# Kernel tuning notes

Measured on AMD Instinct MI355X. Metric: run time of the kernel, lower is better.

Reference implementation:

```python
import jax, jax.numpy as jnp
import numpy as np

N = 4096
IN_F = 512
OUT_F = 64
N_HEADS = 8
ALPHA = 0.2
NEG_INF = -9e15


def setup_inputs() -> dict:
    key = jax.random.key(0)
    k1, k2, k3, k4 = jax.random.split(key, 4)
    h = jax.random.normal(k1, (N, IN_F), dtype=jnp.float32)
    adj = jax.random.randint(k2, (N, N), 0, 2, dtype=jnp.int32)
    W = jax.random.normal(k3, (IN_F, OUT_F * N_HEADS), dtype=jnp.float32) * (1.414 / np.sqrt(IN_F))
    a = jax.random.normal(k4, (2 * OUT_F, 1), dtype=jnp.float32) * 0.1
    return {"h": h, "adj": adj, "W": W, "a": a}


def reference(h, adj, W, a):
    # Wh: [N, H, F]
    Wh = (h @ W).reshape(N, N_HEADS, OUT_F)
    # The all-pairs concat + matmul with a ([2F,1], shared across heads)
    # decomposes exactly: e[i,j,h] = leakyrelu(Wh[i,h]@a[:F] + Wh[j,h]@a[F:])
    a_src = a[:OUT_F, 0]
    a_dst = a[OUT_F:, 0]
    src = jnp.einsum('nhf,f->nh', Wh, a_src)  # [N, H]
    dst = jnp.einsum('nhf,f->nh', Wh, a_dst)  # [N, H]
    e = src[:, None, :] + dst[None, :, :]      # [N, N, H]
    e = jnp.where(e > 0, e, ALPHA * e)         # leaky relu
    e = jnp.where(adj[:, :, None] > 0, e, NEG_INF)
    attention = jax.nn.softmax(e, axis=1)      # softmax over neighbors j
    h_prime = jnp.einsum('ijh,jhf->ihf', attention, Wh)  # [N, H, F]
    out = h_prime.reshape(N, N_HEADS * OUT_F)
    return jax.nn.elu(out)
```

## Files before the change

### kernel.cpp

```cpp
#include <hip/hip_runtime.h>
#include <hip/hip_bf16.h>


typedef unsigned short ushort_t;
typedef __attribute__((ext_vector_type(8))) short bf16x8;
typedef __attribute__((ext_vector_type(4))) float f32x4;

#define LOG2E 1.4426950408889634f

__device__ __forceinline__ ushort_t f2bf(float x) {
    unsigned u = __builtin_bit_cast(unsigned, x);
    u += 0x7FFFu + ((u >> 16) & 1u);
    return (ushort_t)(u >> 16);
}

__global__ __launch_bounds__(256) void transpose_w(const float* __restrict__ W,
                                                   ushort_t* __restrict__ WT) {
    __shared__ ushort_t t[32][33];
    int bx = blockIdx.x & 15, by = blockIdx.x >> 4;
    int tx = threadIdx.x & 31, ty = threadIdx.x >> 5;
#pragma unroll
    for (int i = 0; i < 32; i += 8)
        t[ty + i][tx] = f2bf(W[(by * 32 + ty + i) * 512 + bx * 32 + tx]);
    __syncthreads();
#pragma unroll
    for (int i = 0; i < 32; i += 8)
        WT[(bx * 32 + ty + i) * 512 + by * 32 + tx] = t[tx][ty + i];
}

__global__ __launch_bounds__(256, 4) void gemm_pack(const ushort_t* __restrict__ WT,
                                                    const float* __restrict__ h,
                                                    const float* __restrict__ a,
                                                    ushort_t* __restrict__ WhT,
                                                    float* __restrict__ expA,
                                                    float* __restrict__ expC,
                                                    float* __restrict__ expB,
                                                    float* __restrict__ expD,
                                                    const int* __restrict__ adj,
                                                    unsigned char* __restrict__ pk) {
    __shared__ __align__(16) ushort_t Al[2][64][72];
    __shared__ __align__(16) ushort_t Bl[2][64][72];
    __shared__ float asrc[64], adst[64];
    __shared__ float sred[2][4][64];
    int tid = threadIdx.x;
    if (blockIdx.x >= 512) {
        int pbid = blockIdx.x - 512;
        int wv = tid >> 6, lane = tid & 63;
        int row = pbid * 4 + wv;
        const int* ap = adj + (unsigned)row * 4096 + lane;
        unsigned char* pp = pk + (unsigned)row * 512;
        int g = lane;
        int sv = ((g >> 2) & 1) * 4 + (g & 3);
        int cpar = g >> 3;
#pragma unroll 2
        for (int t = 0; t < 8; t++) {
            unsigned long long m[8];
#pragma unroll
            for (int c8 = 0; c8 < 8; c8++)
                m[c8] = __ballot(ap[(t * 8 + c8) * 64] > 0);
            if (lane < 16) {
                unsigned w = 0;
#pragma unroll
                for (int kq = 0; kq < 4; kq++) {
                    unsigned b = (unsigned)(m[2 * kq + cpar] >> (8 * sv)) & 0xFFu;
                    w |= b << (8 * kq);
                }
                *(unsigned*)(pp + g * 32 + t * 4) = w;
            }
        }
        return;
    }
    int wave = tid >> 6, lane = tid & 63, quad = lane >> 4, nn = lane & 15;
    int mb = blockIdx.x & 7, nb = blockIdx.x >> 3;
    if (tid < 64) {
        asrc[tid] = a[tid] * LOG2E;
        adst[tid] = a[64 + tid] * LOG2E;
    }
    int r = tid >> 2, s0 = tid & 3;
    const ushort_t* Ag = WT + (unsigned)((mb * 64 + r) * 512 + s0 * 8);
    const float* Bg = h + (unsigned)((nb * 64 + r) * 512 + s0 * 8);
    bf16x8 pA0 = *(const bf16x8*)(Ag);
    bf16x8 pA1 = *(const bf16x8*)(Ag + 32);
    float4 pb0 = *(const float4*)(Bg);
    float4 pb1 = *(const float4*)(Bg + 4);
    float4 pb2 = *(const float4*)(Bg + 32);
    float4 pb3 = *(const float4*)(Bg + 36);
    f32x4 acc[4] = {};
#pragma unroll 2
    for (int t = 0; t < 8; t++) {
        int cb = t & 1;
        *(bf16x8*)&Al[cb][r][s0 * 8] = pA0;
        *(bf16x8*)&Al[cb][r][s0 * 8 + 32] = pA1;
        bf16x8 bv;
        bv[0] = (short)f2bf(pb0.x); bv[1] = (short)f2bf(pb0.y);
        bv[2] = (short)f2bf(pb0.z); bv[3] = (short)f2bf(pb0.w);
        bv[4] = (short)f2bf(pb1.x); bv[5] = (short)f2bf(pb1.y);
        bv[6] = (short)f2bf(pb1.z); bv[7] = (short)f2bf(pb1.w);
        *(bf16x8*)&Bl[cb][r][s0 * 8] = bv;
        bv[0] = (short)f2bf(pb2.x); bv[1] = (short)f2bf(pb2.y);
        bv[2] = (short)f2bf(pb2.z); bv[3] = (short)f2bf(pb2.w);
        bv[4] = (short)f2bf(pb3.x); bv[5] = (short)f2bf(pb3.y);
        bv[6] = (short)f2bf(pb3.z); bv[7] = (short)f2bf(pb3.w);
        *(bf16x8*)&Bl[cb][r][s0 * 8 + 32] = bv;
        if (t < 7) {
            int ko = (t + 1) * 64;
            pA0 = *(const bf16x8*)(Ag + ko);
            pA1 = *(const bf16x8*)(Ag + ko + 32);
            pb0 = *(const float4*)(Bg + ko);
            pb1 = *(const float4*)(Bg + ko + 4);
            pb2 = *(const float4*)(Bg + ko + 32);
            pb3 = *(const float4*)(Bg + ko + 36);
        }
        if (t > 0) {
            int pb = cb ^ 1;
            bf16x8 af0 = *(const bf16x8*)&Al[pb][wave * 16 + nn][quad * 8];
            bf16x8 af1 = *(const bf16x8*)&Al[pb][wave * 16 + nn][32 + quad * 8];
#pragma unroll
            for (int nt = 0; nt < 4; nt++) {
                bf16x8 b0 = *(const bf16x8*)&Bl[pb][nt * 16 + nn][quad * 8];
                bf16x8 b1 = *(const bf16x8*)&Bl[pb][nt * 16 + nn][32 + quad * 8];
                acc[nt] = __builtin_amdgcn_mfma_f32_16x16x32_bf16(af0, b0, acc[nt], 0, 0, 0);
                acc[nt] = __builtin_amdgcn_mfma_f32_16x16x32_bf16(af1, b1, acc[nt], 0, 0, 0);
            }
        }
        __syncthreads();
    }
    {
        bf16x8 af0 = *(const bf16x8*)&Al[1][wave * 16 + nn][quad * 8];
        bf16x8 af1 = *(const bf16x8*)&Al[1][wave * 16 + nn][32 + quad * 8];
#pragma unroll
        for (int nt = 0; nt < 4; nt++) {
            bf16x8 b0 = *(const bf16x8*)&Bl[1][nt * 16 + nn][quad * 8];
            bf16x8 b1 = *(const bf16x8*)&Bl[1][nt * 16 + nn][32 + quad * 8];
            acc[nt] = __builtin_amdgcn_mfma_f32_16x16x32_bf16(af0, b0, acc[nt], 0, 0, 0);
            acc[nt] = __builtin_amdgcn_mfma_f32_16x16x32_bf16(af1, b1, acc[nt], 0, 0, 0);
        }
    }
    int row0 = mb * 64 + wave * 16 + quad * 4;
    int col0 = nb * 64 + nn;
    int f0i = wave * 16 + quad * 4;
#pragma unroll
    for (int nt = 0; nt < 4; nt++) {
        float s = 0.f, d = 0.f;
#pragma unroll
        for (int rr = 0; rr < 4; rr++) {
            float v = acc[nt][rr];
            WhT[(unsigned)((row0 + rr) * 4096 + col0 + nt * 16)] = f2bf(v);
            s += v * asrc[f0i + rr];
            d += v * adst[f0i + rr];
        }
        s += __shfl_xor(s, 16); s += __shfl_xor(s, 32);
        d += __shfl_xor(d, 16); d += __shfl_xor(d, 32);
        if (quad == 0) { sred[0][wave][nt * 16 + nn] = s; sred[1][wave][nt * 16 + nn] = d; }
    }
    __syncthreads();
    if (tid < 64) {
        float s = sred[0][0][tid] + sred[0][1][tid] + sred[0][2][tid] + sred[0][3][tid];
        unsigned idx = mb * 4096 + nb * 64 + tid;
        expA[idx] = __builtin_amdgcn_exp2f(s);
        expC[idx] = __builtin_amdgcn_exp2f(0.2f * s);
    } else if (tid < 128) {
        int c = tid - 64;
        float d = sred[1][0][c] + sred[1][1][c] + sred[1][2][c] + sred[1][3][c];
        unsigned idx = mb * 4096 + nb * 64 + c;
        expB[idx] = __builtin_amdgcn_exp2f(d);
        expD[idx] = __builtin_amdgcn_exp2f(0.2f * d);
    }
}

__global__ __launch_bounds__(512, 4) void gat_attn(const unsigned char* __restrict__ pk,
                                                   const ushort_t* __restrict__ WhT,
                                                   const float* __restrict__ expA,
                                                   const float* __restrict__ expC,
                                                   const float* __restrict__ expB,
                                                   const float* __restrict__ expD,
                                                   float* __restrict__ out) {
    __shared__ __align__(16) ushort_t Vb[2][128][144];
    __shared__ float denomp[4][2][32];
    int tid = threadIdx.x;
    int wave = tid >> 6, lane = tid & 63, quad = lane >> 4, nn = lane & 15;
    int hb = blockIdx.x >> 7, ib = blockIdx.x & 127;
    int i0 = ib * 32;
    int whead = wave & 1, jq = wave >> 1;
    int g = jq * 4 + quad;
    int head = hb * 2 + whead;
    float Ai0 = expA[head * 4096 + i0 + nn];
    float Ci0 = expC[head * 4096 + i0 + nn];
    float Ai1 = expA[head * 4096 + i0 + 16 + nn];
    float Ci1 = expC[head * 4096 + i0 + 16 + nn];
    const unsigned char* mpA = pk + (unsigned)(i0 + nn) * 512 + g * 32;
    const unsigned char* mpB = mpA + 16 * 512;
    const float* Bp = expB + (unsigned)head * 4096 + jq * 32 + quad * 8;
    const float* Dp = expD + (unsigned)head * 4096 + jq * 32 + quad * 8;
    int vrow = tid >> 2, vs = tid & 3;
    const ushort_t* Vg = WhT + (unsigned)(hb * 128 + vrow) * 4096 + vs * 8;
    bf16x8 onef;
#pragma unroll
    for (int i = 0; i < 8; i++) onef[i] = (short)0x3F80;
    f32x4 acc[2][4] = {};
    f32x4 accd[2] = {};
    bf16x8 pv[4];
    float4 pBD[4];
    pv[0] = *(const bf16x8*)(Vg);
    pv[1] = *(const bf16x8*)(Vg + 32);
    pv[2] = *(const bf16x8*)(Vg + 64);
    pv[3] = *(const bf16x8*)(Vg + 96);
    pBD[0] = *(const float4*)(Bp);
    pBD[1] = *(const float4*)(Bp + 4);
    pBD[2] = *(const float4*)(Dp);
    pBD[3] = *(const float4*)(Dp + 4);
    unsigned mcA = *(const unsigned*)(mpA);
    unsigned mcB = *(const unsigned*)(mpB);
    unsigned mnA = 0, mnB = 0;
    for (int t = 0; t < 8; t++) {
#pragma unroll
        for (int u = 0; u < 4; u++) {
            int kb = t * 4 + u;
            int cb = kb & 1;
            *(bf16x8*)&Vb[cb][vrow][vs * 8] = pv[0];
            *(bf16x8*)&Vb[cb][vrow][vs * 8 + 32] = pv[1];
            *(bf16x8*)&Vb[cb][vrow][vs * 8 + 64] = pv[2];
            *(bf16x8*)&Vb[cb][vrow][vs * 8 + 96] = pv[3];
            float4 Bv0 = pBD[0], Bv1 = pBD[1], Dv0 = pBD[2], Dv1 = pBD[3];
            bf16x8 af0, af1;
            {
                unsigned w0, w1, w2, w3, w4, w5, w6, w7;
                float w;
                w = fmaxf(Ai0 * Bv0.x, Ci0 * Dv0.x);
                w0 = __builtin_bit_cast(unsigned, w) & 0xFFFF0000u;
                w0 &= (unsigned)__builtin_amdgcn_sbfe(mcA, u * 8 + 0, 1);
                w = fmaxf(Ai0 * Bv0.y, Ci0 * Dv0.y);
                w1 = __builtin_bit_cast(unsigned, w) & 0xFFFF0000u;
                w1 &= (unsigned)__builtin_amdgcn_sbfe(mcA, u * 8 + 1, 1);
                w = fmaxf(Ai0 * Bv0.z, Ci0 * Dv0.z);
                w2 = __builtin_bit_cast(unsigned, w) & 0xFFFF0000u;
                w2 &= (unsigned)__builtin_amdgcn_sbfe(mcA, u * 8 + 2, 1);
                w = fmaxf(Ai0 * Bv0.w, Ci0 * Dv0.w);
                w3 = __builtin_bit_cast(unsigned, w) & 0xFFFF0000u;
                w3 &= (unsigned)__builtin_amdgcn_sbfe(mcA, u * 8 + 3, 1);
                w = fmaxf(Ai0 * Bv1.x, Ci0 * Dv1.x);
                w4 = __builtin_bit_cast(unsigned, w) & 0xFFFF0000u;
                w4 &= (unsigned)__builtin_amdgcn_sbfe(mcA, u * 8 + 4, 1);
                w = fmaxf(Ai0 * Bv1.y, Ci0 * Dv1.y);
                w5 = __builtin_bit_cast(unsigned, w) & 0xFFFF0000u;
                w5 &= (unsigned)__builtin_amdgcn_sbfe(mcA, u * 8 + 5, 1);
                w = fmaxf(Ai0 * Bv1.z, Ci0 * Dv1.z);
                w6 = __builtin_bit_cast(unsigned, w) & 0xFFFF0000u;
                w6 &= (unsigned)__builtin_amdgcn_sbfe(mcA, u * 8 + 6, 1);
                w = fmaxf(Ai0 * Bv1.w, Ci0 * Dv1.w);
                w7 = __builtin_bit_cast(unsigned, w) & 0xFFFF0000u;
                w7 &= (unsigned)__builtin_amdgcn_sbfe(mcA, u * 8 + 7, 1);
                uint4 pq;
                pq.x = __builtin_amdgcn_perm(w1, w0, 0x07060302u);
                pq.y = __builtin_amdgcn_perm(w3, w2, 0x07060302u);
                pq.z = __builtin_amdgcn_perm(w5, w4, 0x07060302u);
                pq.w = __builtin_amdgcn_perm(w7, w6, 0x07060302u);
                af0 = __builtin_bit_cast(bf16x8, pq);
                w = fmaxf(Ai1 * Bv0.x, Ci1 * Dv0.x);
                w0 = __builtin_bit_cast(unsigned, w) & 0xFFFF0000u;
                w0 &= (unsigned)__builtin_amdgcn_sbfe(mcB, u * 8 + 0, 1);
                w = fmaxf(Ai1 * Bv0.y, Ci1 * Dv0.y);
                w1 = __builtin_bit_cast(unsigned, w) & 0xFFFF0000u;
                w1 &= (unsigned)__builtin_amdgcn_sbfe(mcB, u * 8 + 1, 1);
                w = fmaxf(Ai1 * Bv0.z, Ci1 * Dv0.z);
                w2 = __builtin_bit_cast(unsigned, w) & 0xFFFF0000u;
                w2 &= (unsigned)__builtin_amdgcn_sbfe(mcB, u * 8 + 2, 1);
                w = fmaxf(Ai1 * Bv0.w, Ci1 * Dv0.w);
                w3 = __builtin_bit_cast(unsigned, w) & 0xFFFF0000u;
                w3 &= (unsigned)__builtin_amdgcn_sbfe(mcB, u * 8 + 3, 1);
                w = fmaxf(Ai1 * Bv1.x, Ci1 * Dv1.x);
                w4 = __builtin_bit_cast(unsigned, w) & 0xFFFF0000u;
                w4 &= (unsigned)__builtin_amdgcn_sbfe(mcB, u * 8 + 4, 1);
                w = fmaxf(Ai1 * Bv1.y, Ci1 * Dv1.y);
                w5 = __builtin_bit_cast(unsigned, w) & 0xFFFF0000u;
                w5 &= (unsigned)__builtin_amdgcn_sbfe(mcB, u * 8 + 5, 1);
                w = fmaxf(Ai1 * Bv1.z, Ci1 * Dv1.z);
                w6 = __builtin_bit_cast(unsigned, w) & 0xFFFF0000u;
                w6 &= (unsigned)__builtin_amdgcn_sbfe(mcB, u * 8 + 6, 1);
                w = fmaxf(Ai1 * Bv1.w, Ci1 * Dv1.w);
                w7 = __builtin_bit_cast(unsigned, w) & 0xFFFF0000u;
                w7 &= (unsigned)__builtin_amdgcn_sbfe(mcB, u * 8 + 7, 1);
                pq.x = __builtin_amdgcn_perm(w1, w0, 0x07060302u);
                pq.y = __builtin_amdgcn_perm(w3, w2, 0x07060302u);
                pq.z = __builtin_amdgcn_perm(w5, w4, 0x07060302u);
                pq.w = __builtin_amdgcn_perm(w7, w6, 0x07060302u);
                af1 = __builtin_bit_cast(bf16x8, pq);
            }
            if (u == 3) { mcA = mnA; mcB = mnB; }
            __syncthreads();
            __builtin_amdgcn_sched_barrier(0);
            if (kb < 31) {
                const ushort_t* vp = Vg + (kb + 1) * 128;
                pv[0] = *(const bf16x8*)(vp);
                pv[1] = *(const bf16x8*)(vp + 32);
                pv[2] = *(const bf16x8*)(vp + 64);
                pv[3] = *(const bf16x8*)(vp + 96);
                pBD[0] = *(const float4*)(Bp + (kb + 1) * 128);
                pBD[1] = *(const float4*)(Bp + (kb + 1) * 128 + 4);
                pBD[2] = *(const float4*)(Dp + (kb + 1) * 128);
                pBD[3] = *(const float4*)(Dp + (kb + 1) * 128 + 4);
            }
            if (u == 0 && t < 7) {
                mnA = *(const unsigned*)(mpA + (t + 1) * 4);
                mnB = *(const unsigned*)(mpB + (t + 1) * 4);
            }
#pragma unroll
            for (int nt = 0; nt < 4; nt++) {
                bf16x8 bv = *(const bf16x8*)&Vb[cb][whead * 64 + nt * 16 + nn][jq * 32 + quad * 8];
                acc[0][nt] = __builtin_amdgcn_mfma_f32_16x16x32_bf16(af0, bv, acc[0][nt], 0, 0, 0);
                acc[1][nt] = __builtin_amdgcn_mfma_f32_16x16x32_bf16(af1, bv, acc[1][nt], 0, 0, 0);
            }
            accd[0] = __builtin_amdgcn_mfma_f32_16x16x32_bf16(af0, onef, accd[0], 0, 0, 0);
            accd[1] = __builtin_amdgcn_mfma_f32_16x16x32_bf16(af1, onef, accd[1], 0, 0, 0);
        }
    }
    __syncthreads();
    if (nn == 0) {
#pragma unroll
        for (int s = 0; s < 2; s++)
#pragma unroll
            for (int rr = 0; rr < 4; rr++)
                denomp[jq][whead][s * 16 + quad * 4 + rr] = accd[s][rr];
    }
    float (*cmb)[3][64][32] = reinterpret_cast<float (*)[3][64][32]>(&Vb[0][0][0]);
    if (jq > 0) {
#pragma unroll
        for (int s = 0; s < 2; s++)
#pragma unroll
            for (int nt = 0; nt < 4; nt++)
                *(f32x4*)&cmb[whead][jq - 1][lane][s * 16 + nt * 4] = acc[s][nt];
    }
    __syncthreads();
    if (jq == 0) {
#pragma unroll
        for (int s = 0; s < 2; s++) {
#pragma unroll
            for (int nt = 0; nt < 4; nt++) {
                f32x4 o = acc[s][nt]
                        + *(const f32x4*)&cmb[whead][0][lane][s * 16 + nt * 4]
                        + *(const f32x4*)&cmb[whead][1][lane][s * 16 + nt * 4]
                        + *(const f32x4*)&cmb[whead][2][lane][s * 16 + nt * 4];
#pragma unroll
                for (int rr = 0; rr < 4; rr++) {
                    int il = s * 16 + quad * 4 + rr;
                    float dnm = fmaxf(denomp[0][whead][il] + denomp[1][whead][il]
                                    + denomp[2][whead][il] + denomp[3][whead][il], 1e-30f);
                    float v = o[rr] / dnm;
                    v = v > 0.f ? v : __expf(v) - 1.f;
                    out[(unsigned)(i0 + il) * 512 + hb * 128 + whead * 64 + nt * 16 + nn] = v;
                }
            }
        }
    }
}

extern "C" void kernel_launch(void* const* d_in, const int* in_sizes, int n_in,
                              void* d_out, int out_size, void* d_ws, size_t ws_size,
                              hipStream_t stream) {
    const float* h   = (const float*)d_in[0];
    const int*   adj = (const int*)d_in[1];
    const float* W   = (const float*)d_in[2];
    const float* a   = (const float*)d_in[3];

    char* ws = (char*)d_ws;
    ushort_t* WhT = (ushort_t*)ws;
    ushort_t* WT  = (ushort_t*)(ws + (4u << 20));
    float* expA = (float*)(ws + (4u << 20) + (512u << 10));
    float* expC = expA + 8 * 4096;
    float* expB = expC + 8 * 4096;
    float* expD = expB + 8 * 4096;
    unsigned char* pkm = (unsigned char*)(ws + (5u << 20));

    transpose_w<<<256, 256, 0, stream>>>(W, WT);
    gemm_pack<<<1536, 256, 0, stream>>>(WT, h, a, WhT, expA, expC, expB, expD,
                                        adj, pkm);
    gat_attn<<<512, 512, 0, stream>>>(pkm, WhT, expA, expC, expB, expD,
                                      (float*)d_out);
}
```

Measured before the change: 169.6 us.

## Pre-swizzle Wh into MFMA fragment layout and load B operands directly from global

The GEMM epilogue now writes Wh in a tiled layout that matches the per-lane B-fragment order of the attention kernel's MFMA. The attention kernel then loads its V fragments straight from global memory. This removes the LDS staging buffer, the per-step __syncthreads, and the software prefetch of V and the exp tables. The trade-off is that global load latency is no longer hidden by explicit double buffering, the epilogue does scattered 2-byte stores, and each wave reads V fragments without sharing them through LDS.

```diff
diff --git a/kernel.cpp b/kernel.cpp
--- a/kernel.cpp
+++ b/kernel.cpp
@@ -31,7 +31,7 @@
 __global__ __launch_bounds__(256, 4) void gemm_pack(const ushort_t* __restrict__ WT,
                                                     const float* __restrict__ h,
                                                     const float* __restrict__ a,
-                                                    ushort_t* __restrict__ WhT,
+                                                    ushort_t* __restrict__ WhTn,
                                                     float* __restrict__ expA,
                                                     float* __restrict__ expC,
                                                     float* __restrict__ expB,
@@ -136,16 +136,18 @@
             acc[nt] = __builtin_amdgcn_mfma_f32_16x16x32_bf16(af1, b1, acc[nt], 0, 0, 0);
         }
     }
-    int row0 = mb * 64 + wave * 16 + quad * 4;
-    int col0 = nb * 64 + nn;
     int f0i = wave * 16 + quad * 4;
 #pragma unroll
     for (int nt = 0; nt < 4; nt++) {
         float s = 0.f, d = 0.f;
+        int c = nb * 64 + nn + nt * 16;
+        int kb = c >> 7, jq = (c >> 5) & 3, qa = (c >> 3) & 3, e = c & 7;
+        unsigned base = (unsigned)(((((mb * 32 + kb) * 4 + jq) * 4 + wave) * 64
+                                    + qa * 16 + quad * 4) * 8 + e);
 #pragma unroll
         for (int rr = 0; rr < 4; rr++) {
             float v = acc[nt][rr];
-            WhT[(unsigned)((row0 + rr) * 4096 + col0 + nt * 16)] = f2bf(v);
+            WhTn[base + rr * 8] = f2bf(v);
             s += v * asrc[f0i + rr];
             d += v * adst[f0i + rr];
         }
@@ -169,13 +171,13 @@
 }
 
 __global__ __launch_bounds__(512, 4) void gat_attn(const unsigned char* __restrict__ pk,
-                                                   const ushort_t* __restrict__ WhT,
+                                                   const ushort_t* __restrict__ WhTn,
                                                    const float* __restrict__ expA,
                                                    const float* __restrict__ expC,
                                                    const float* __restrict__ expB,
                                                    const float* __restrict__ expD,
                                                    float* __restrict__ out) {
-    __shared__ __align__(16) ushort_t Vb[2][128][144];
+    __shared__ float cmb[2][3][64][32];
     __shared__ float denomp[4][2][32];
     int tid = threadIdx.x;
     int wave = tid >> 6, lane = tid & 63, quad = lane >> 4, nn = lane & 15;
@@ -192,36 +194,27 @@
     const unsigned char* mpB = mpA + 16 * 512;
     const float* Bp = expB + (unsigned)head * 4096 + jq * 32 + quad * 8;
     const float* Dp = expD + (unsigned)head * 4096 + jq * 32 + quad * 8;
-    int vrow = tid >> 2, vs = tid & 3;
-    const ushort_t* Vg = WhT + (unsigned)(hb * 128 + vrow) * 4096 + vs * 8;
+    const ushort_t* vb = WhTn + (unsigned)head * 262144u + (unsigned)jq * 2048u + lane * 8;
     bf16x8 onef;
 #pragma unroll
     for (int i = 0; i < 8; i++) onef[i] = (short)0x3F80;
     f32x4 acc[2][4] = {};
     f32x4 accd[2] = {};
-    bf16x8 pv[4];
-    float4 pBD[4];
-    pv[0] = *(const bf16x8*)(Vg);
-    pv[1] = *(const bf16x8*)(Vg + 32);
-    pv[2] = *(const bf16x8*)(Vg + 64);
-    pv[3] = *(const bf16x8*)(Vg + 96);
-    pBD[0] = *(const float4*)(Bp);
-    pBD[1] = *(const float4*)(Bp + 4);
-    pBD[2] = *(const float4*)(Dp);
-    pBD[3] = *(const float4*)(Dp + 4);
-    unsigned mcA = *(const unsigned*)(mpA);
-    unsigned mcB = *(const unsigned*)(mpB);
-    unsigned mnA = 0, mnB = 0;
     for (int t = 0; t < 8; t++) {
+        unsigned mcA = *(const unsigned*)(mpA + t * 4);
+        unsigned mcB = *(const unsigned*)(mpB + t * 4);
 #pragma unroll
         for (int u = 0; u < 4; u++) {
             int kb = t * 4 + u;
-            int cb = kb & 1;
-            *(bf16x8*)&Vb[cb][vrow][vs * 8] = pv[0];
-            *(bf16x8*)&Vb[cb][vrow][vs * 8 + 32] = pv[1];
-            *(bf16x8*)&Vb[cb][vrow][vs * 8 + 64] = pv[2];
-            *(bf16x8*)&Vb[cb][vrow][vs * 8 + 96] = pv[3];
-            float4 Bv0 = pBD[0], Bv1 = pBD[1], Dv0 = pBD[2], Dv1 = pBD[3];
+            const ushort_t* vt = vb + (unsigned)kb * 8192u;
+            bf16x8 v0 = *(const bf16x8*)(vt);
+            bf16x8 v1 = *(const bf16x8*)(vt + 512);
+            bf16x8 v2 = *(const bf16x8*)(vt + 1024);
+            bf16x8 v3 = *(const bf16x8*)(vt + 1536);
+            float4 Bv0 = *(const float4*)(Bp + kb * 128);
+            float4 Bv1 = *(const float4*)(Bp + kb * 128 + 4);
+            float4 Dv0 = *(const float4*)(Dp + kb * 128);
+            float4 Dv1 = *(const float4*)(Dp + kb * 128 + 4);
             bf16x8 af0, af1;
             {
                 unsigned w0, w1, w2, w3, w4, w5, w6, w7;
@@ -286,35 +279,18 @@
                 pq.w = __builtin_amdgcn_perm(w7, w6, 0x07060302u);
                 af1 = __builtin_bit_cast(bf16x8, pq);
             }
-            if (u == 3) { mcA = mnA; mcB = mnB; }
-            __syncthreads();
-            __builtin_amdgcn_sched_barrier(0);
-            if (kb < 31) {
-                const ushort_t* vp = Vg + (kb + 1) * 128;
-                pv[0] = *(const bf16x8*)(vp);
-                pv[1] = *(const bf16x8*)(vp + 32);
-                pv[2] = *(const bf16x8*)(vp + 64);
-                pv[3] = *(const bf16x8*)(vp + 96);
-                pBD[0] = *(const float4*)(Bp + (kb + 1) * 128);
-                pBD[1] = *(const float4*)(Bp + (kb + 1) * 128 + 4);
-                pBD[2] = *(const float4*)(Dp + (kb + 1) * 128);
-                pBD[3] = *(const float4*)(Dp + (kb + 1) * 128 + 4);
-            }
-            if (u == 0 && t < 7) {
-                mnA = *(const unsigned*)(mpA + (t + 1) * 4);
-                mnB = *(const unsigned*)(mpB + (t + 1) * 4);
-            }
-#pragma unroll
-            for (int nt = 0; nt < 4; nt++) {
-                bf16x8 bv = *(const bf16x8*)&Vb[cb][whead * 64 + nt * 16 + nn][jq * 32 + quad * 8];
-                acc[0][nt] = __builtin_amdgcn_mfma_f32_16x16x32_bf16(af0, bv, acc[0][nt], 0, 0, 0);
-                acc[1][nt] = __builtin_amdgcn_mfma_f32_16x16x32_bf16(af1, bv, acc[1][nt], 0, 0, 0);
-            }
+            acc[0][0] = __builtin_amdgcn_mfma_f32_16x16x32_bf16(af0, v0, acc[0][0], 0, 0, 0);
+            acc[1][0] = __builtin_amdgcn_mfma_f32_16x16x32_bf16(af1, v0, acc[1][0], 0, 0, 0);
+            acc[0][1] = __builtin_amdgcn_mfma_f32_16x16x32_bf16(af0, v1, acc[0][1], 0, 0, 0);
+            acc[1][1] = __builtin_amdgcn_mfma_f32_16x16x32_bf16(af1, v1, acc[1][1], 0, 0, 0);
+            acc[0][2] = __builtin_amdgcn_mfma_f32_16x16x32_bf16(af0, v2, acc[0][2], 0, 0, 0);
+            acc[1][2] = __builtin_amdgcn_mfma_f32_16x16x32_bf16(af1, v2, acc[1][2], 0, 0, 0);
+            acc[0][3] = __builtin_amdgcn_mfma_f32_16x16x32_bf16(af0, v3, acc[0][3], 0, 0, 0);
+            acc[1][3] = __builtin_amdgcn_mfma_f32_16x16x32_bf16(af1, v3, acc[1][3], 0, 0, 0);
             accd[0] = __builtin_amdgcn_mfma_f32_16x16x32_bf16(af0, onef, accd[0], 0, 0, 0);
             accd[1] = __builtin_amdgcn_mfma_f32_16x16x32_bf16(af1, onef, accd[1], 0, 0, 0);
         }
     }
-    __syncthreads();
     if (nn == 0) {
 #pragma unroll
         for (int s = 0; s < 2; s++)
@@ -322,7 +298,6 @@
             for (int rr = 0; rr < 4; rr++)
                 denomp[jq][whead][s * 16 + quad * 4 + rr] = accd[s][rr];
     }
-    float (*cmb)[3][64][32] = reinterpret_cast<float (*)[3][64][32]>(&Vb[0][0][0]);
     if (jq > 0) {
 #pragma unroll
         for (int s = 0; s < 2; s++)
@@ -363,8 +338,8 @@
     const float* a   = (const float*)d_in[3];
 
     char* ws = (char*)d_ws;
-    ushort_t* WhT = (ushort_t*)ws;
-    ushort_t* WT  = (ushort_t*)(ws + (4u << 20));
+    ushort_t* WhTn = (ushort_t*)ws;
+    ushort_t* WT   = (ushort_t*)(ws + (4u << 20));
     float* expA = (float*)(ws + (4u << 20) + (512u << 10));
     float* expC = expA + 8 * 4096;
     float* expB = expC + 8 * 4096;
@@ -372,8 +347,8 @@
     unsigned char* pkm = (unsigned char*)(ws + (5u << 20));
 
     transpose_w<<<256, 256, 0, stream>>>(W, WT);
-    gemm_pack<<<1536, 256, 0, stream>>>(WT, h, a, WhT, expA, expC, expB, expD,
+    gemm_pack<<<1536, 256, 0, stream>>>(WT, h, a, WhTn, expA, expC, expB, expD,
                                         adj, pkm);
-    gat_attn<<<512, 512, 0, stream>>>(pkm, WhT, expA, expC, expB, expD,
+    gat_attn<<<512, 512, 0, stream>>>(pkm, WhTn, expA, expC, expB, expD,
                                       (float*)d_out);
 }
```

After: 172.5 us. About the same (+1.7%).
